# Kernel optimization log

Hardware: AMD Instinct MI355X
Metric: run time of the kernel (lower is better)

The kernel has to match this reference:

```python
import jax, jax.numpy as jnp
from jax import lax
import numpy as np

D_MODEL = 512
MODES = 16
B, S = 8, 4096
EPS = 1e-5


def setup_inputs() -> dict:
    key = jax.random.key(0)
    ks = jax.random.split(key, 7)
    x = jax.random.normal(ks[0], (B, S, D_MODEL), dtype=jnp.float32)
    gamma = jnp.ones((D_MODEL,), dtype=jnp.float32)
    beta = jnp.zeros((D_MODEL,), dtype=jnp.float32)
    # complex spectral weights stored as real/imag parts, torch init: randn(cfloat)*0.02
    wr = jax.random.normal(ks[1], (D_MODEL, MODES), dtype=jnp.float32) * 0.02
    wi = jax.random.normal(ks[2], (D_MODEL, MODES), dtype=jnp.float32) * 0.02
    # Conv1d(d_model, d_model, 3): weight (out, in, k), torch default uniform(-b, b)
    bound = 1.0 / np.sqrt(D_MODEL * 3)
    conv_w = jax.random.uniform(ks[3], (D_MODEL, D_MODEL, 3), dtype=jnp.float32, minval=-bound, maxval=bound)
    conv_b = jax.random.uniform(ks[4], (D_MODEL,), dtype=jnp.float32, minval=-bound, maxval=bound)
    return {"x": x, "gamma": gamma, "beta": beta, "wr": wr, "wi": wi,
            "conv_w": conv_w, "conv_b": conv_b}


def reference(x, gamma, beta, wr, wi, conv_w, conv_b):
    Bq, Sq, Dq = x.shape
    residual = x
    # LayerNorm over last dim (biased variance, eps=1e-5)
    mu = jnp.mean(x, axis=-1, keepdims=True)
    var = jnp.var(x, axis=-1, keepdims=True)
    xn = (x - mu) * lax.rsqrt(var + EPS) * gamma + beta
    # truncated-mode spectral conv: rfft along seq, multiply first `modes` bins, irfft
    xf = jnp.fft.rfft(xn, axis=1, norm='ortho')           # [B, S//2+1, D] complex
    m = min(wr.shape[1], xf.shape[1])
    w = (wr + 1j * wi).T[:m]                              # [m, D]
    out_ft = jnp.zeros_like(xf).at[:, :m, :].set(xf[:, :m, :] * w[None])
    xs = jnp.fft.irfft(out_ft, n=Sq, axis=1, norm='ortho')  # [B, S, D] real
    # Conv1d(k=3, pad=1) over seq dim on channel-first layout
    xc = lax.conv_general_dilated(
        xs.transpose(0, 2, 1), conv_w, window_strides=(1,), padding=[(1, 1)],
        dimension_numbers=('NCH', 'OIH', 'NCH'))
    xc = (xc + conv_b[None, :, None]).transpose(0, 2, 1)
    return residual + xs + xc
```

## Files before the change

kernel.cpp:

```cpp
#include <hip/hip_runtime.h>
#include <hip/hip_bf16.h>
#include <math.h>

#define Bn 8
#define Sn 4096
#define Dn 512
#define MODES 16
#define ANGF 0.0015339807878856412f

#define PART_OFF 0
#define Y_OFF 8388608
#define WTF_OFF 8519680
#define ZP_OFF 9306112
#define G_OFF 10878976
#define V_OFF 11010048
#define STATS_OFF 11018240

__global__ __launch_bounds__(256) void k_transpose_w(
    const float* __restrict__ cw, float* __restrict__ wTf) {
  int idx = blockIdx.x * 256 + threadIdx.x;
  int o = idx & 511;
  int d = (idx >> 9) & 511;
  int t = idx >> 18;
  wTf[idx] = cw[o * 1536 + d * 3 + t];
}

__global__ __launch_bounds__(256) void k_stats(const float* __restrict__ x,
                                               float2* __restrict__ stats) {
  int wave = threadIdx.x >> 6, lane = threadIdx.x & 63;
  int row0 = blockIdx.x * 32 + wave * 8;
  for (int j = 0; j < 8; ++j) {
    int row = row0 + j;
    const float4* px = (const float4*)(x + ((size_t)row << 9));
    float4 v0 = px[lane * 2];
    float4 v1 = px[lane * 2 + 1];
    float ps = v0.x + v0.y + v0.z + v0.w + v1.x + v1.y + v1.z + v1.w;
    float pq = v0.x * v0.x + v0.y * v0.y + v0.z * v0.z + v0.w * v0.w +
               v1.x * v1.x + v1.y * v1.y + v1.z * v1.z + v1.w * v1.w;
#pragma unroll
    for (int off = 32; off > 0; off >>= 1) {
      ps += __shfl_down(ps, off);
      pq += __shfl_down(pq, off);
    }
    if (lane == 0) {
      float mu = ps * (1.0f / Dn);
      float var = pq * (1.0f / Dn) - mu * mu;
      stats[row] = make_float2(mu, rsqrtf(var + 1e-5f));
    }
  }
}

__global__ __launch_bounds__(256) void k_project(
    const float* __restrict__ x, const float* __restrict__ gamma,
    const float* __restrict__ beta, const float2* __restrict__ stats,
    float* __restrict__ partials) {
  int blk = blockIdx.x;
  int b = blk >> 6;
  int c = blk & 63;
  int tid = threadIdx.x;
  int d0 = tid << 1;
  int s_base = c << 4;

  __shared__ __attribute__((aligned(16))) float2 s_tw[16][MODES];
  __shared__ float2 s_mv[64];
  {
    int r = tid >> 4, k = tid & 15;
    int m = ((s_base + r) * k) & (Sn - 1);
    float sn, cn;
    __sincosf((float)m * ANGF, &sn, &cn);
    s_tw[r][k] = make_float2(cn, sn);
    if (tid < 64) {
      s_mv[tid] = stats[(b << 12) + ((tid >> 4) << 10) + s_base + (tid & 15)];
    }
  }
  __syncthreads();

  float2 g = *(const float2*)(gamma + d0);
  float2 be = *(const float2*)(beta + d0);

  float2 accRe[MODES], accIm[MODES];
#pragma unroll
  for (int k = 0; k < MODES; k++) {
    accRe[k] = make_float2(0.f, 0.f);
    accIm[k] = make_float2(0.f, 0.f);
  }

  const float* xb = x + (((size_t)b << 12) << 9) + d0;
  float2 cur[4], nxt[4];
#pragma unroll
  for (int j = 0; j < 4; ++j)
    cur[j] = *(const float2*)(xb + ((size_t)((j << 10) + s_base) << 9));

#pragma unroll 2
  for (int r = 0; r < 16; ++r) {
    if (r < 15) {
#pragma unroll
      for (int j = 0; j < 4; ++j)
        nxt[j] =
            *(const float2*)(xb + ((size_t)((j << 10) + s_base + r + 1) << 9));
    }
    float2 xn[4];
#pragma unroll
    for (int j = 0; j < 4; ++j) {
      float2 mv = s_mv[(j << 4) + r];
      float ax = mv.y * g.x, ay = mv.y * g.y;
      xn[j] = make_float2((cur[j].x - mv.x) * ax + be.x,
                          (cur[j].y - mv.x) * ay + be.y);
    }
    float2 t02p = make_float2(xn[0].x + xn[2].x, xn[0].y + xn[2].y);
    float2 t02m = make_float2(xn[0].x - xn[2].x, xn[0].y - xn[2].y);
    float2 t13p = make_float2(xn[1].x + xn[3].x, xn[1].y + xn[3].y);
    float2 t13m = make_float2(xn[1].x - xn[3].x, xn[1].y - xn[3].y);
    float2 u0 = make_float2(t02p.x + t13p.x, t02p.y + t13p.y);
    float2 u1 = make_float2(t02p.x - t13p.x, t02p.y - t13p.y);

    const float4* twr = (const float4*)&s_tw[r][0];
#pragma unroll
    for (int kk = 0; kk < 8; ++kk) {
      float4 t2 = twr[kk];
      const int k0 = 2 * kk, k1 = 2 * kk + 1;
      {
        float2 u = ((k0 & 3) == 0) ? u0 : u1;
        accRe[k0].x += u.x * t2.x;
        accRe[k0].y += u.y * t2.x;
        accIm[k0].x -= u.x * t2.y;
        accIm[k0].y -= u.y * t2.y;
      }
      if ((k1 & 3) == 1) {
        accRe[k1].x += t2.z * t02m.x - t2.w * t13m.x;
        accRe[k1].y += t2.z * t02m.y - t2.w * t13m.y;
        accIm[k1].x -= t2.z * t13m.x + t2.w * t02m.x;
        accIm[k1].y -= t2.z * t13m.y + t2.w * t02m.y;
      } else {
        accRe[k1].x += t2.z * t02m.x + t2.w * t13m.x;
        accRe[k1].y += t2.z * t02m.y + t2.w * t13m.y;
        accIm[k1].x += t2.z * t13m.x - t2.w * t02m.x;
        accIm[k1].y += t2.z * t13m.y - t2.w * t02m.y;
      }
    }
#pragma unroll
    for (int j = 0; j < 4; ++j) cur[j] = nxt[j];
  }

  size_t base = ((size_t)(b * 64 + c)) * MODES;
  float4* P4 = (float4*)partials;
#pragma unroll
  for (int k = 0; k < MODES; k++)
    P4[(base + k) * 256 + tid] =
        make_float4(accRe[k].x, accIm[k].x, accRe[k].y, accIm[k].y);
}

__global__ __launch_bounds__(256) void k_reduce_modes(
    const float* __restrict__ partials, const float* __restrict__ wr,
    const float* __restrict__ wi, float* __restrict__ Y) {
  int idx = blockIdx.x * 256 + threadIdx.x;
  int d = idx & 511;
  int k = (idx >> 9) & 15;
  int b = idx >> 13;
  const float2* P = (const float2*)partials;
  float re = 0.f, im = 0.f;
#pragma unroll 8
  for (int c = 0; c < 64; c++) {
    float2 p = P[(((size_t)(b * 64 + c)) * MODES + k) * Dn + d];
    re += p.x;
    im += p.y;
  }
  float wrv = wr[d * MODES + k];
  float wiv = wi[d * MODES + k];
  float yre = re * wrv - im * wiv;
  float yim = re * wiv + im * wrv;
  float scale = (k == 0) ? (1.0f / 4096.0f) : (2.0f / 4096.0f);
  ((float2*)Y)[((size_t)b * MODES + k) * Dn + d] =
      make_float2(yre * scale, yim * scale);
}

__global__ __launch_bounds__(256) void k_build_z(
    const float* __restrict__ Y, const float* __restrict__ wTf,
    float* __restrict__ Zp) {
  int blk = blockIdx.x;
  int b = blk / 96;
  int rem = blk % 96;
  int t = rem >> 5;
  int r2 = rem & 31;
  int och = r2 >> 2;
  int dch = r2 & 3;
  int tid = threadIdx.x;
  int oi = tid & 63, kq = tid >> 6;
  int o = och * 64 + oi;
  int d0 = dch * 128;

  __shared__ float2 Ys[MODES][128];
  const float2* Y2 = (const float2*)Y;
#pragma unroll
  for (int i = 0; i < 8; i++) {
    int e = tid + i * 256;
    int k = e >> 7, dd = e & 127;
    Ys[k][dd] = Y2[(((size_t)(b * MODES + k)) << 9) + d0 + dd];
  }
  __syncthreads();

  float zc[4] = {0.f, 0.f, 0.f, 0.f}, zs[4] = {0.f, 0.f, 0.f, 0.f};
  const float* wp = wTf + (((size_t)(t * Dn + d0)) << 9) + o;
  float wv_n = wp[0];
  for (int dd = 0; dd < 128; ++dd) {
    float wv = wv_n;
    if (dd < 127) wv_n = wp[(size_t)(dd + 1) << 9];
#pragma unroll
    for (int m = 0; m < 4; m++) {
      float2 y = Ys[kq * 4 + m][dd];
      zc[m] += y.x * wv;
      zs[m] += y.y * wv;
    }
  }
  float2* Z2 = (float2*)Zp;
#pragma unroll
  for (int m = 0; m < 4; m++) {
    int k = kq * 4 + m;
    Z2[(((size_t)(dch * 24 + b * 3 + t) * MODES + k)) << 9 | o] =
        make_float2(zc[m], zs[m]);
  }
}

__global__ __launch_bounds__(256) void k_build_g(
    const float* __restrict__ Y, const float* __restrict__ Zp,
    float* __restrict__ G, float* __restrict__ V) {
  int idx = blockIdx.x * 256 + threadIdx.x;
  const float2* Y2 = (const float2*)Y;
  const float2* Z2 = (const float2*)Zp;
  if (idx < 65536) {
    int o = idx & 511;
    int k = (idx >> 9) & 15;
    int b = idx >> 13;
    float2 z0 = make_float2(0.f, 0.f), z1 = z0, z2 = z0;
#pragma unroll
    for (int dch = 0; dch < 4; dch++) {
      float2 a0 = Z2[(((size_t)(dch * 24 + b * 3 + 0) * MODES + k)) << 9 | o];
      float2 a1 = Z2[(((size_t)(dch * 24 + b * 3 + 1) * MODES + k)) << 9 | o];
      float2 a2 = Z2[(((size_t)(dch * 24 + b * 3 + 2) * MODES + k)) << 9 | o];
      z0.x += a0.x; z0.y += a0.y;
      z1.x += a1.x; z1.y += a1.y;
      z2.x += a2.x; z2.y += a2.y;
    }
    float2 y = Y2[(((size_t)(b * MODES + k)) << 9) + o];
    float sf, cf;
    __sincosf((float)k * ANGF, &sf, &cf);
    float gc = y.x + (cf * z0.x + sf * z0.y) + z1.x + (cf * z2.x - sf * z2.y);
    float gs = y.y + (cf * z0.y - sf * z0.x) + z1.y + (cf * z2.y + sf * z2.x);
    G[(((size_t)(b * MODES + k) * 2 + 0)) << 9 | o] = gc;
    G[(((size_t)(b * MODES + k) * 2 + 1)) << 9 | o] = gs;
  } else if (idx < 65536 + 8192) {
    int j = idx - 65536;
    int o = j & 511;
    int comp = (j >> 9) & 1;
    int b = j >> 10;
    float v = 0.f;
#pragma unroll
    for (int k = 0; k < MODES; k++) {
      float2 z = make_float2(0.f, 0.f);
#pragma unroll
      for (int dch = 0; dch < 4; dch++) {
        float2 a = Z2[(((size_t)(dch * 24 + b * 3 + (comp ? 2 : 0)) * MODES +
                        k)) << 9 | o];
        z.x += a.x; z.y += a.y;
      }
      if (comp == 0) {
        float sf, cf;
        __sincosf((float)k * ANGF, &sf, &cf);
        v += cf * z.x + sf * z.y;
      } else {
        v += z.x;
      }
    }
    V[((size_t)(b * 2 + comp) << 9) + o] = v;
  }
}

__global__ __launch_bounds__(256) void k_apply(
    const float* __restrict__ x, const float* __restrict__ G,
    const float* __restrict__ V, const float* __restrict__ conv_b,
    float* __restrict__ out) {
  int b = blockIdx.x >> 7;
  int rt = blockIdx.x & 127;
  int r0 = rt << 3;
  int tid = threadIdx.x;
  int o0 = tid << 1;

  __shared__ __attribute__((aligned(16))) float2 s_tw[8][MODES];
  if (tid < 128) {
    int rr = tid >> 4, k = tid & 15;
    int m = ((r0 + rr) * k) & (Sn - 1);
    float sn, cn;
    __sincosf((float)m * ANGF, &sn, &cn);
    s_tw[rr][k] = make_float2(cn, sn);
  }

  float2 Gc[MODES], Gs[MODES];
  const float2* Gp = (const float2*)(G + ((size_t)b * MODES * 2 * Dn));
#pragma unroll
  for (int k = 0; k < MODES; k++) {
    Gc[k] = Gp[(k * 2 + 0) * 256 + tid];
    Gs[k] = Gp[(k * 2 + 1) * 256 + tid];
  }
  float2 cb2 = *(const float2*)&conv_b[o0];
  __syncthreads();

  const float* xb = x + (((size_t)b << 12) << 9) + o0;
  float* ob = out + (((size_t)b << 12) << 9) + o0;

  float2 cur[4], nxt[4];
#pragma unroll
  for (int j = 0; j < 4; ++j)
    cur[j] = *(const float2*)(xb + ((size_t)((j << 10) + r0) << 9));

#pragma unroll 2
  for (int rr = 0; rr < 8; ++rr) {
    if (rr < 7) {
#pragma unroll
      for (int j = 0; j < 4; ++j)
        nxt[j] = *(const float2*)(xb + ((size_t)((j << 10) + r0 + rr + 1) << 9));
    }
    float2 a0 = make_float2(0.f, 0.f), a1 = a0, a2 = a0, a3 = a0;
    const float4* twr = (const float4*)&s_tw[rr][0];
#pragma unroll
    for (int kk = 0; kk < 8; ++kk) {
      float4 t2 = twr[kk];
#define APPLY_K(kidx, cc, ss)                                          \
  {                                                                    \
    float2 Pre = make_float2(cc * Gc[kidx].x - ss * Gs[kidx].x,        \
                             cc * Gc[kidx].y - ss * Gs[kidx].y);       \
    float2 Pim = make_float2(cc * Gs[kidx].x + ss * Gc[kidx].x,        \
                             cc * Gs[kidx].y + ss * Gc[kidx].y);       \
    a0.x += Pre.x; a0.y += Pre.y;                                      \
    if (((kidx) & 3) == 0) {                                           \
      a1.x += Pre.x; a1.y += Pre.y;                                    \
      a2.x += Pre.x; a2.y += Pre.y;                                    \
      a3.x += Pre.x; a3.y += Pre.y;                                    \
    } else if (((kidx) & 3) == 1) {                                    \
      a1.x -= Pim.x; a1.y -= Pim.y;                                    \
      a2.x -= Pre.x; a2.y -= Pre.y;                                    \
      a3.x += Pim.x; a3.y += Pim.y;                                    \
    } else if (((kidx) & 3) == 2) {                                    \
      a1.x -= Pre.x; a1.y -= Pre.y;                                    \
      a2.x += Pre.x; a2.y += Pre.y;                                    \
      a3.x -= Pre.x; a3.y -= Pre.y;                                    \
    } else {                                                           \
      a1.x += Pim.x; a1.y += Pim.y;                                    \
      a2.x -= Pre.x; a2.y -= Pre.y;                                    \
      a3.x -= Pim.x; a3.y -= Pim.y;                                    \
    }                                                                  \
  }
      APPLY_K(2 * kk, t2.x, t2.y);
      APPLY_K(2 * kk + 1, t2.z, t2.w);
#undef APPLY_K
    }
    int s_r = r0 + rr;
#pragma unroll
    for (int j = 0; j < 4; ++j) {
      float2 aj = (j == 0) ? a0 : (j == 1) ? a1 : (j == 2) ? a2 : a3;
      int s = s_r + (j << 10);
      float2 o2 = make_float2(cur[j].x + cb2.x + aj.x,
                              cur[j].y + cb2.y + aj.y);
      if (s == 0) {
        float2 v = *(const float2*)&V[((size_t)(b * 2 + 0) << 9) + o0];
        o2.x -= v.x; o2.y -= v.y;
      }
      if (s == Sn - 1) {
        float2 v = *(const float2*)&V[((size_t)(b * 2 + 1) << 9) + o0];
        o2.x -= v.x; o2.y -= v.y;
      }
      *(float2*)(ob + ((size_t)s << 9)) = o2;
    }
#pragma unroll
    for (int j = 0; j < 4; ++j) cur[j] = nxt[j];
  }
}

extern "C" void kernel_launch(void* const* d_in, const int* in_sizes, int n_in,
                              void* d_out, int out_size, void* d_ws,
                              size_t ws_size, hipStream_t stream) {
  const float* x = (const float*)d_in[0];
  const float* gamma = (const float*)d_in[1];
  const float* beta = (const float*)d_in[2];
  const float* wr = (const float*)d_in[3];
  const float* wi = (const float*)d_in[4];
  const float* conv_w = (const float*)d_in[5];
  const float* conv_b = (const float*)d_in[6];
  float* out = (float*)d_out;

  float* ws = (float*)d_ws;
  float* partials = ws + PART_OFF;
  float* Y = ws + Y_OFF;
  float* wTf = ws + WTF_OFF;
  float* Zp = ws + ZP_OFF;
  float* G = ws + G_OFF;
  float* V = ws + V_OFF;
  float2* stats = (float2*)(ws + STATS_OFF);

  hipLaunchKernelGGL(k_transpose_w, dim3(3072), dim3(256), 0, stream, conv_w,
                     wTf);
  hipLaunchKernelGGL(k_stats, dim3(1024), dim3(256), 0, stream, x, stats);
  hipLaunchKernelGGL(k_project, dim3(512), dim3(256), 0, stream, x, gamma,
                     beta, stats, partials);
  hipLaunchKernelGGL(k_reduce_modes, dim3(256), dim3(256), 0, stream, partials,
                     wr, wi, Y);
  hipLaunchKernelGGL(k_build_z, dim3(768), dim3(256), 0, stream, Y, wTf, Zp);
  hipLaunchKernelGGL(k_build_g, dim3(288), dim3(256), 0, stream, Y, Zp, G, V);
  hipLaunchKernelGGL(k_apply, dim3(1024), dim3(256), 0, stream, x, G, V,
                     conv_b, out);
}
```

Before: 190.2 us.

## Fuse LayerNorm stats into projection and merge middle stages into cooperative kernel

Computes per-row LayerNorm mean and rstd inside k_project rather than in a separate k_stats pass. The weight transpose, mode reduction, Z build and G/V build are merged into one cooperative kernel that uses grid.sync between phases. This drops four kernel launches and one extra read of x, in exchange for grid-wide barriers and a cooperative launch of 768 blocks that must all be co-resident.

```diff
diff --git a/kernel.cpp b/kernel.cpp
--- a/kernel.cpp
+++ b/kernel.cpp
@@ -1,6 +1,9 @@
 #include <hip/hip_runtime.h>
 #include <hip/hip_bf16.h>
+#include <hip/hip_cooperative_groups.h>
 #include <math.h>
+
+namespace cg = cooperative_groups;
 
 #define Bn 8
 #define Sn 4096
@@ -14,46 +17,10 @@
 #define ZP_OFF 9306112
 #define G_OFF 10878976
 #define V_OFF 11010048
-#define STATS_OFF 11018240
-
-__global__ __launch_bounds__(256) void k_transpose_w(
-    const float* __restrict__ cw, float* __restrict__ wTf) {
-  int idx = blockIdx.x * 256 + threadIdx.x;
-  int o = idx & 511;
-  int d = (idx >> 9) & 511;
-  int t = idx >> 18;
-  wTf[idx] = cw[o * 1536 + d * 3 + t];
-}
-
-__global__ __launch_bounds__(256) void k_stats(const float* __restrict__ x,
-                                               float2* __restrict__ stats) {
-  int wave = threadIdx.x >> 6, lane = threadIdx.x & 63;
-  int row0 = blockIdx.x * 32 + wave * 8;
-  for (int j = 0; j < 8; ++j) {
-    int row = row0 + j;
-    const float4* px = (const float4*)(x + ((size_t)row << 9));
-    float4 v0 = px[lane * 2];
-    float4 v1 = px[lane * 2 + 1];
-    float ps = v0.x + v0.y + v0.z + v0.w + v1.x + v1.y + v1.z + v1.w;
-    float pq = v0.x * v0.x + v0.y * v0.y + v0.z * v0.z + v0.w * v0.w +
-               v1.x * v1.x + v1.y * v1.y + v1.z * v1.z + v1.w * v1.w;
-#pragma unroll
-    for (int off = 32; off > 0; off >>= 1) {
-      ps += __shfl_down(ps, off);
-      pq += __shfl_down(pq, off);
-    }
-    if (lane == 0) {
-      float mu = ps * (1.0f / Dn);
-      float var = pq * (1.0f / Dn) - mu * mu;
-      stats[row] = make_float2(mu, rsqrtf(var + 1e-5f));
-    }
-  }
-}
 
 __global__ __launch_bounds__(256) void k_project(
     const float* __restrict__ x, const float* __restrict__ gamma,
-    const float* __restrict__ beta, const float2* __restrict__ stats,
-    float* __restrict__ partials) {
+    const float* __restrict__ beta, float* __restrict__ partials) {
   int blk = blockIdx.x;
   int b = blk >> 6;
   int c = blk & 63;
@@ -63,14 +30,44 @@
 
   __shared__ __attribute__((aligned(16))) float2 s_tw[16][MODES];
   __shared__ float2 s_mv[64];
+
   {
     int r = tid >> 4, k = tid & 15;
     int m = ((s_base + r) * k) & (Sn - 1);
     float sn, cn;
     __sincosf((float)m * ANGF, &sn, &cn);
     s_tw[r][k] = make_float2(cn, sn);
-    if (tid < 64) {
-      s_mv[tid] = stats[(b << 12) + ((tid >> 4) << 10) + s_base + (tid & 15)];
+  }
+
+  {
+    int w = tid >> 6, lane = tid & 63;
+    const float4* px = (const float4*)(
+        x + (((size_t)((b << 12) + (w << 10) + s_base)) << 9));
+#pragma unroll
+    for (int rg = 0; rg < 16; rg += 4) {
+      float4 v[8];
+#pragma unroll
+      for (int q = 0; q < 4; ++q) {
+        v[2 * q] = px[(rg + q) * 128 + lane * 2];
+        v[2 * q + 1] = px[(rg + q) * 128 + lane * 2 + 1];
+      }
+#pragma unroll
+      for (int q = 0; q < 4; ++q) {
+        float4 v0 = v[2 * q], v1 = v[2 * q + 1];
+        float ps = v0.x + v0.y + v0.z + v0.w + v1.x + v1.y + v1.z + v1.w;
+        float pq = v0.x * v0.x + v0.y * v0.y + v0.z * v0.z + v0.w * v0.w +
+                   v1.x * v1.x + v1.y * v1.y + v1.z * v1.z + v1.w * v1.w;
+#pragma unroll
+        for (int off = 32; off > 0; off >>= 1) {
+          ps += __shfl_down(ps, off);
+          pq += __shfl_down(pq, off);
+        }
+        if (lane == 0) {
+          float mu = ps * (1.0f / Dn);
+          float var = pq * (1.0f / Dn) - mu * mu;
+          s_mv[w * 16 + rg + q] = make_float2(mu, rsqrtf(var + 1e-5f));
+        }
+      }
     }
   }
   __syncthreads();
@@ -150,128 +147,146 @@
         make_float4(accRe[k].x, accIm[k].x, accRe[k].y, accIm[k].y);
 }
 
-__global__ __launch_bounds__(256) void k_reduce_modes(
+__global__ __launch_bounds__(256, 3) void k_mid(
+    const float* __restrict__ cw, float* __restrict__ wTf,
     const float* __restrict__ partials, const float* __restrict__ wr,
-    const float* __restrict__ wi, float* __restrict__ Y) {
-  int idx = blockIdx.x * 256 + threadIdx.x;
-  int d = idx & 511;
-  int k = (idx >> 9) & 15;
-  int b = idx >> 13;
-  const float2* P = (const float2*)partials;
-  float re = 0.f, im = 0.f;
-#pragma unroll 8
-  for (int c = 0; c < 64; c++) {
-    float2 p = P[(((size_t)(b * 64 + c)) * MODES + k) * Dn + d];
-    re += p.x;
-    im += p.y;
-  }
-  float wrv = wr[d * MODES + k];
-  float wiv = wi[d * MODES + k];
-  float yre = re * wrv - im * wiv;
-  float yim = re * wiv + im * wrv;
-  float scale = (k == 0) ? (1.0f / 4096.0f) : (2.0f / 4096.0f);
-  ((float2*)Y)[((size_t)b * MODES + k) * Dn + d] =
-      make_float2(yre * scale, yim * scale);
-}
-
-__global__ __launch_bounds__(256) void k_build_z(
-    const float* __restrict__ Y, const float* __restrict__ wTf,
-    float* __restrict__ Zp) {
+    const float* __restrict__ wi, float* __restrict__ Y,
+    float* __restrict__ Zp, float* __restrict__ G, float* __restrict__ V) {
+  cg::grid_group grid = cg::this_grid();
   int blk = blockIdx.x;
-  int b = blk / 96;
-  int rem = blk % 96;
-  int t = rem >> 5;
-  int r2 = rem & 31;
-  int och = r2 >> 2;
-  int dch = r2 & 3;
   int tid = threadIdx.x;
-  int oi = tid & 63, kq = tid >> 6;
-  int o = och * 64 + oi;
-  int d0 = dch * 128;
 
   __shared__ float2 Ys[MODES][128];
-  const float2* Y2 = (const float2*)Y;
-#pragma unroll
-  for (int i = 0; i < 8; i++) {
-    int e = tid + i * 256;
-    int k = e >> 7, dd = e & 127;
-    Ys[k][dd] = Y2[(((size_t)(b * MODES + k)) << 9) + d0 + dd];
-  }
-  __syncthreads();
-
-  float zc[4] = {0.f, 0.f, 0.f, 0.f}, zs[4] = {0.f, 0.f, 0.f, 0.f};
-  const float* wp = wTf + (((size_t)(t * Dn + d0)) << 9) + o;
-  float wv_n = wp[0];
-  for (int dd = 0; dd < 128; ++dd) {
-    float wv = wv_n;
-    if (dd < 127) wv_n = wp[(size_t)(dd + 1) << 9];
-#pragma unroll
-    for (int m = 0; m < 4; m++) {
-      float2 y = Ys[kq * 4 + m][dd];
-      zc[m] += y.x * wv;
-      zs[m] += y.y * wv;
-    }
-  }
-  float2* Z2 = (float2*)Zp;
-#pragma unroll
-  for (int m = 0; m < 4; m++) {
-    int k = kq * 4 + m;
-    Z2[(((size_t)(dch * 24 + b * 3 + t) * MODES + k)) << 9 | o] =
-        make_float2(zc[m], zs[m]);
-  }
-}
-
-__global__ __launch_bounds__(256) void k_build_g(
-    const float* __restrict__ Y, const float* __restrict__ Zp,
-    float* __restrict__ G, float* __restrict__ V) {
-  int idx = blockIdx.x * 256 + threadIdx.x;
-  const float2* Y2 = (const float2*)Y;
-  const float2* Z2 = (const float2*)Zp;
-  if (idx < 65536) {
-    int o = idx & 511;
+
+  {
+    int base0 = blk << 10;
+#pragma unroll
+    for (int u = 0; u < 4; ++u) {
+      int idx = base0 + (u << 8) + tid;
+      int o = idx & 511;
+      int d = (idx >> 9) & 511;
+      int t = idx >> 18;
+      wTf[idx] = cw[o * 1536 + d * 3 + t];
+    }
+  }
+  if (blk < 256) {
+    int idx = (blk << 8) + tid;
+    int d = idx & 511;
     int k = (idx >> 9) & 15;
     int b = idx >> 13;
-    float2 z0 = make_float2(0.f, 0.f), z1 = z0, z2 = z0;
-#pragma unroll
-    for (int dch = 0; dch < 4; dch++) {
-      float2 a0 = Z2[(((size_t)(dch * 24 + b * 3 + 0) * MODES + k)) << 9 | o];
-      float2 a1 = Z2[(((size_t)(dch * 24 + b * 3 + 1) * MODES + k)) << 9 | o];
-      float2 a2 = Z2[(((size_t)(dch * 24 + b * 3 + 2) * MODES + k)) << 9 | o];
-      z0.x += a0.x; z0.y += a0.y;
-      z1.x += a1.x; z1.y += a1.y;
-      z2.x += a2.x; z2.y += a2.y;
-    }
-    float2 y = Y2[(((size_t)(b * MODES + k)) << 9) + o];
-    float sf, cf;
-    __sincosf((float)k * ANGF, &sf, &cf);
-    float gc = y.x + (cf * z0.x + sf * z0.y) + z1.x + (cf * z2.x - sf * z2.y);
-    float gs = y.y + (cf * z0.y - sf * z0.x) + z1.y + (cf * z2.y + sf * z2.x);
-    G[(((size_t)(b * MODES + k) * 2 + 0)) << 9 | o] = gc;
-    G[(((size_t)(b * MODES + k) * 2 + 1)) << 9 | o] = gs;
-  } else if (idx < 65536 + 8192) {
-    int j = idx - 65536;
-    int o = j & 511;
-    int comp = (j >> 9) & 1;
-    int b = j >> 10;
-    float v = 0.f;
-#pragma unroll
-    for (int k = 0; k < MODES; k++) {
-      float2 z = make_float2(0.f, 0.f);
+    const float2* P = (const float2*)partials;
+    float re = 0.f, im = 0.f;
+#pragma unroll 8
+    for (int c = 0; c < 64; c++) {
+      float2 p = P[(((size_t)(b * 64 + c)) * MODES + k) * Dn + d];
+      re += p.x;
+      im += p.y;
+    }
+    float wrv = wr[d * MODES + k];
+    float wiv = wi[d * MODES + k];
+    float yre = re * wrv - im * wiv;
+    float yim = re * wiv + im * wrv;
+    float scale = (k == 0) ? (1.0f / 4096.0f) : (2.0f / 4096.0f);
+    ((float2*)Y)[((size_t)b * MODES + k) * Dn + d] =
+        make_float2(yre * scale, yim * scale);
+  }
+
+  grid.sync();
+
+  {
+    int b = blk / 96;
+    int rem = blk % 96;
+    int t = rem >> 5;
+    int r2 = rem & 31;
+    int och = r2 >> 2;
+    int dch = r2 & 3;
+    int oi = tid & 63, kq = tid >> 6;
+    int o = och * 64 + oi;
+    int d0 = dch * 128;
+
+    const float2* Y2 = (const float2*)Y;
+#pragma unroll
+    for (int i = 0; i < 8; i++) {
+      int e = tid + i * 256;
+      int k = e >> 7, dd = e & 127;
+      Ys[k][dd] = Y2[(((size_t)(b * MODES + k)) << 9) + d0 + dd];
+    }
+    __syncthreads();
+
+    float zc[4] = {0.f, 0.f, 0.f, 0.f}, zs[4] = {0.f, 0.f, 0.f, 0.f};
+    const float* wp = wTf + (((size_t)(t * Dn + d0)) << 9) + o;
+    float wv_n = wp[0];
+    for (int dd = 0; dd < 128; ++dd) {
+      float wv = wv_n;
+      if (dd < 127) wv_n = wp[(size_t)(dd + 1) << 9];
+#pragma unroll
+      for (int m = 0; m < 4; m++) {
+        float2 y = Ys[kq * 4 + m][dd];
+        zc[m] += y.x * wv;
+        zs[m] += y.y * wv;
+      }
+    }
+    float2* Z2 = (float2*)Zp;
+#pragma unroll
+    for (int m = 0; m < 4; m++) {
+      int k = kq * 4 + m;
+      Z2[(((size_t)(dch * 24 + b * 3 + t) * MODES + k)) << 9 | o] =
+          make_float2(zc[m], zs[m]);
+    }
+  }
+
+  grid.sync();
+
+  {
+    int idx = (blk << 8) + tid;
+    const float2* Y2 = (const float2*)Y;
+    const float2* Z2 = (const float2*)Zp;
+    if (idx < 65536) {
+      int o = idx & 511;
+      int k = (idx >> 9) & 15;
+      int b = idx >> 13;
+      float2 z0 = make_float2(0.f, 0.f), z1 = z0, z2 = z0;
 #pragma unroll
       for (int dch = 0; dch < 4; dch++) {
-        float2 a = Z2[(((size_t)(dch * 24 + b * 3 + (comp ? 2 : 0)) * MODES +
-                        k)) << 9 | o];
-        z.x += a.x; z.y += a.y;
-      }
-      if (comp == 0) {
-        float sf, cf;
-        __sincosf((float)k * ANGF, &sf, &cf);
-        v += cf * z.x + sf * z.y;
-      } else {
-        v += z.x;
-      }
-    }
-    V[((size_t)(b * 2 + comp) << 9) + o] = v;
+        float2 a0 = Z2[(((size_t)(dch * 24 + b * 3 + 0) * MODES + k)) << 9 | o];
+        float2 a1 = Z2[(((size_t)(dch * 24 + b * 3 + 1) * MODES + k)) << 9 | o];
+        float2 a2 = Z2[(((size_t)(dch * 24 + b * 3 + 2) * MODES + k)) << 9 | o];
+        z0.x += a0.x; z0.y += a0.y;
+        z1.x += a1.x; z1.y += a1.y;
+        z2.x += a2.x; z2.y += a2.y;
+      }
+      float2 y = Y2[(((size_t)(b * MODES + k)) << 9) + o];
+      float sf, cf;
+      __sincosf((float)k * ANGF, &sf, &cf);
+      float gc = y.x + (cf * z0.x + sf * z0.y) + z1.x + (cf * z2.x - sf * z2.y);
+      float gs = y.y + (cf * z0.y - sf * z0.x) + z1.y + (cf * z2.y + sf * z2.x);
+      G[(((size_t)(b * MODES + k) * 2 + 0)) << 9 | o] = gc;
+      G[(((size_t)(b * MODES + k) * 2 + 1)) << 9 | o] = gs;
+    } else if (idx < 65536 + 8192) {
+      int j = idx - 65536;
+      int o = j & 511;
+      int comp = (j >> 9) & 1;
+      int b = j >> 10;
+      float v = 0.f;
+#pragma unroll
+      for (int k = 0; k < MODES; k++) {
+        float2 z = make_float2(0.f, 0.f);
+#pragma unroll
+        for (int dch = 0; dch < 4; dch++) {
+          float2 a = Z2[(((size_t)(dch * 24 + b * 3 + (comp ? 2 : 0)) * MODES +
+                          k)) << 9 | o];
+          z.x += a.x; z.y += a.y;
+        }
+        if (comp == 0) {
+          float sf, cf;
+          __sincosf((float)k * ANGF, &sf, &cf);
+          v += cf * z.x + sf * z.y;
+        } else {
+          v += z.x;
+        }
+      }
+      V[((size_t)(b * 2 + comp) << 9) + o] = v;
+    }
   }
 }
 
@@ -394,17 +409,27 @@
   float* Zp = ws + ZP_OFF;
   float* G = ws + G_OFF;
   float* V = ws + V_OFF;
-  float2* stats = (float2*)(ws + STATS_OFF);
-
-  hipLaunchKernelGGL(k_transpose_w, dim3(3072), dim3(256), 0, stream, conv_w,
-                     wTf);
-  hipLaunchKernelGGL(k_stats, dim3(1024), dim3(256), 0, stream, x, stats);
+
   hipLaunchKernelGGL(k_project, dim3(512), dim3(256), 0, stream, x, gamma,
-                     beta, stats, partials);
-  hipLaunchKernelGGL(k_reduce_modes, dim3(256), dim3(256), 0, stream, partials,
-                     wr, wi, Y);
-  hipLaunchKernelGGL(k_build_z, dim3(768), dim3(256), 0, stream, Y, wTf, Zp);
-  hipLaunchKernelGGL(k_build_g, dim3(288), dim3(256), 0, stream, Y, Zp, G, V);
+                     beta, partials);
+
+  {
+    const float* cw_a = conv_w;
+    float* wTf_a = wTf;
+    const float* part_a = partials;
+    const float* wr_a = wr;
+    const float* wi_a = wi;
+    float* Y_a = Y;
+    float* Zp_a = Zp;
+    float* G_a = G;
+    float* V_a = V;
+    void* args[] = {(void*)&cw_a, (void*)&wTf_a, (void*)&part_a,
+                    (void*)&wr_a, (void*)&wi_a,  (void*)&Y_a,
+                    (void*)&Zp_a, (void*)&G_a,   (void*)&V_a};
+    hipLaunchCooperativeKernel((const void*)k_mid, dim3(768), dim3(256), args,
+                               0, stream);
+  }
+
   hipLaunchKernelGGL(k_apply, dim3(1024), dim3(256), 0, stream, x, G, V,
                      conv_b, out);
 }
```

After: 376.8 us. +98.1%, slower.

## Fuse stats, weight transpose and G-build into neighbouring kernels

Applied to the files above, without the earlier changes.

Folds the LayerNorm statistics into k_project, which now computes the mean and rstd of its own 64 rows from x instead of reading a separate stats buffer. Extra blocks in k_project also do the conv weight transpose. k_build_z now loops over all four d-chunks itself, so it writes a single Z with no partials. The G and V build moves into k_apply, which computes them from Y and Z in registers. Together this cuts the launch count from seven to four and drops one full read pass over x, at the cost of fewer blocks in build_z and redundant G computation in every k_apply block.

```diff
diff --git a/kernel.cpp b/kernel.cpp
--- a/kernel.cpp
+++ b/kernel.cpp
@@ -11,66 +11,73 @@
 #define PART_OFF 0
 #define Y_OFF 8388608
 #define WTF_OFF 8519680
-#define ZP_OFF 9306112
-#define G_OFF 10878976
-#define V_OFF 11010048
-#define STATS_OFF 11018240
-
-__global__ __launch_bounds__(256) void k_transpose_w(
-    const float* __restrict__ cw, float* __restrict__ wTf) {
-  int idx = blockIdx.x * 256 + threadIdx.x;
-  int o = idx & 511;
-  int d = (idx >> 9) & 511;
-  int t = idx >> 18;
-  wTf[idx] = cw[o * 1536 + d * 3 + t];
-}
-
-__global__ __launch_bounds__(256) void k_stats(const float* __restrict__ x,
-                                               float2* __restrict__ stats) {
-  int wave = threadIdx.x >> 6, lane = threadIdx.x & 63;
-  int row0 = blockIdx.x * 32 + wave * 8;
-  for (int j = 0; j < 8; ++j) {
-    int row = row0 + j;
-    const float4* px = (const float4*)(x + ((size_t)row << 9));
-    float4 v0 = px[lane * 2];
-    float4 v1 = px[lane * 2 + 1];
-    float ps = v0.x + v0.y + v0.z + v0.w + v1.x + v1.y + v1.z + v1.w;
-    float pq = v0.x * v0.x + v0.y * v0.y + v0.z * v0.z + v0.w * v0.w +
-               v1.x * v1.x + v1.y * v1.y + v1.z * v1.z + v1.w * v1.w;
-#pragma unroll
-    for (int off = 32; off > 0; off >>= 1) {
-      ps += __shfl_down(ps, off);
-      pq += __shfl_down(pq, off);
-    }
-    if (lane == 0) {
-      float mu = ps * (1.0f / Dn);
-      float var = pq * (1.0f / Dn) - mu * mu;
-      stats[row] = make_float2(mu, rsqrtf(var + 1e-5f));
-    }
-  }
-}
+#define Z_OFF 9306112
 
 __global__ __launch_bounds__(256) void k_project(
     const float* __restrict__ x, const float* __restrict__ gamma,
-    const float* __restrict__ beta, const float2* __restrict__ stats,
-    float* __restrict__ partials) {
+    const float* __restrict__ beta, const float* __restrict__ cw,
+    float* __restrict__ wTf, float* __restrict__ partials) {
   int blk = blockIdx.x;
+  int tid = threadIdx.x;
+
+  if (blk >= 512) {
+    int base0 = (blk - 512) * 3072;
+#pragma unroll
+    for (int u = 0; u < 12; ++u) {
+      int idx = base0 + (u << 8) + tid;
+      int o = idx & 511;
+      int d = (idx >> 9) & 511;
+      int t = idx >> 18;
+      wTf[idx] = cw[o * 1536 + d * 3 + t];
+    }
+    return;
+  }
+
   int b = blk >> 6;
   int c = blk & 63;
-  int tid = threadIdx.x;
   int d0 = tid << 1;
   int s_base = c << 4;
 
   __shared__ __attribute__((aligned(16))) float2 s_tw[16][MODES];
   __shared__ float2 s_mv[64];
+
   {
     int r = tid >> 4, k = tid & 15;
     int m = ((s_base + r) * k) & (Sn - 1);
     float sn, cn;
     __sincosf((float)m * ANGF, &sn, &cn);
     s_tw[r][k] = make_float2(cn, sn);
-    if (tid < 64) {
-      s_mv[tid] = stats[(b << 12) + ((tid >> 4) << 10) + s_base + (tid & 15)];
+  }
+
+  {
+    int w = tid >> 6, lane = tid & 63;
+    const float4* px = (const float4*)(
+        x + (((size_t)((b << 12) + (w << 10) + s_base)) << 9));
+#pragma unroll
+    for (int rg = 0; rg < 16; rg += 4) {
+      float4 v[8];
+#pragma unroll
+      for (int q = 0; q < 4; ++q) {
+        v[2 * q] = px[(rg + q) * 128 + lane * 2];
+        v[2 * q + 1] = px[(rg + q) * 128 + lane * 2 + 1];
+      }
+#pragma unroll
+      for (int q = 0; q < 4; ++q) {
+        float4 v0 = v[2 * q], v1 = v[2 * q + 1];
+        float ps = v0.x + v0.y + v0.z + v0.w + v1.x + v1.y + v1.z + v1.w;
+        float pq = v0.x * v0.x + v0.y * v0.y + v0.z * v0.z + v0.w * v0.w +
+                   v1.x * v1.x + v1.y * v1.y + v1.z * v1.z + v1.w * v1.w;
+#pragma unroll
+        for (int off = 32; off > 0; off >>= 1) {
+          ps += __shfl_down(ps, off);
+          pq += __shfl_down(pq, off);
+        }
+        if (lane == 0) {
+          float mu = ps * (1.0f / Dn);
+          float var = pq * (1.0f / Dn) - mu * mu;
+          s_mv[w * 16 + rg + q] = make_float2(mu, rsqrtf(var + 1e-5f));
+        }
+      }
     }
   }
   __syncthreads();
@@ -176,108 +183,57 @@
 
 __global__ __launch_bounds__(256) void k_build_z(
     const float* __restrict__ Y, const float* __restrict__ wTf,
-    float* __restrict__ Zp) {
+    float* __restrict__ Z) {
   int blk = blockIdx.x;
-  int b = blk / 96;
-  int rem = blk % 96;
-  int t = rem >> 5;
-  int r2 = rem & 31;
-  int och = r2 >> 2;
-  int dch = r2 & 3;
+  int b = blk / 24;
+  int rem = blk % 24;
+  int t = rem >> 3;
+  int och = rem & 7;
   int tid = threadIdx.x;
   int oi = tid & 63, kq = tid >> 6;
   int o = och * 64 + oi;
-  int d0 = dch * 128;
 
   __shared__ float2 Ys[MODES][128];
   const float2* Y2 = (const float2*)Y;
-#pragma unroll
-  for (int i = 0; i < 8; i++) {
-    int e = tid + i * 256;
-    int k = e >> 7, dd = e & 127;
-    Ys[k][dd] = Y2[(((size_t)(b * MODES + k)) << 9) + d0 + dd];
-  }
-  __syncthreads();
 
   float zc[4] = {0.f, 0.f, 0.f, 0.f}, zs[4] = {0.f, 0.f, 0.f, 0.f};
-  const float* wp = wTf + (((size_t)(t * Dn + d0)) << 9) + o;
-  float wv_n = wp[0];
-  for (int dd = 0; dd < 128; ++dd) {
-    float wv = wv_n;
-    if (dd < 127) wv_n = wp[(size_t)(dd + 1) << 9];
-#pragma unroll
-    for (int m = 0; m < 4; m++) {
-      float2 y = Ys[kq * 4 + m][dd];
-      zc[m] += y.x * wv;
-      zs[m] += y.y * wv;
-    }
-  }
-  float2* Z2 = (float2*)Zp;
+  for (int dch = 0; dch < 4; ++dch) {
+    int d0 = dch * 128;
+#pragma unroll
+    for (int i = 0; i < 8; i++) {
+      int e = tid + i * 256;
+      int k = e >> 7, dd = e & 127;
+      Ys[k][dd] = Y2[(((size_t)(b * MODES + k)) << 9) + d0 + dd];
+    }
+    __syncthreads();
+
+    const float* wp = wTf + (((size_t)(t * Dn + d0)) << 9) + o;
+    float wv_n = wp[0];
+    for (int dd = 0; dd < 128; ++dd) {
+      float wv = wv_n;
+      if (dd < 127) wv_n = wp[(size_t)(dd + 1) << 9];
+#pragma unroll
+      for (int m = 0; m < 4; m++) {
+        float2 y = Ys[kq * 4 + m][dd];
+        zc[m] += y.x * wv;
+        zs[m] += y.y * wv;
+      }
+    }
+    __syncthreads();
+  }
+
+  float2* Z2 = (float2*)Z;
 #pragma unroll
   for (int m = 0; m < 4; m++) {
     int k = kq * 4 + m;
-    Z2[(((size_t)(dch * 24 + b * 3 + t) * MODES + k)) << 9 | o] =
+    Z2[(((size_t)((b * 3 + t) * MODES + k)) << 9) + o] =
         make_float2(zc[m], zs[m]);
   }
 }
 
-__global__ __launch_bounds__(256) void k_build_g(
-    const float* __restrict__ Y, const float* __restrict__ Zp,
-    float* __restrict__ G, float* __restrict__ V) {
-  int idx = blockIdx.x * 256 + threadIdx.x;
-  const float2* Y2 = (const float2*)Y;
-  const float2* Z2 = (const float2*)Zp;
-  if (idx < 65536) {
-    int o = idx & 511;
-    int k = (idx >> 9) & 15;
-    int b = idx >> 13;
-    float2 z0 = make_float2(0.f, 0.f), z1 = z0, z2 = z0;
-#pragma unroll
-    for (int dch = 0; dch < 4; dch++) {
-      float2 a0 = Z2[(((size_t)(dch * 24 + b * 3 + 0) * MODES + k)) << 9 | o];
-      float2 a1 = Z2[(((size_t)(dch * 24 + b * 3 + 1) * MODES + k)) << 9 | o];
-      float2 a2 = Z2[(((size_t)(dch * 24 + b * 3 + 2) * MODES + k)) << 9 | o];
-      z0.x += a0.x; z0.y += a0.y;
-      z1.x += a1.x; z1.y += a1.y;
-      z2.x += a2.x; z2.y += a2.y;
-    }
-    float2 y = Y2[(((size_t)(b * MODES + k)) << 9) + o];
-    float sf, cf;
-    __sincosf((float)k * ANGF, &sf, &cf);
-    float gc = y.x + (cf * z0.x + sf * z0.y) + z1.x + (cf * z2.x - sf * z2.y);
-    float gs = y.y + (cf * z0.y - sf * z0.x) + z1.y + (cf * z2.y + sf * z2.x);
-    G[(((size_t)(b * MODES + k) * 2 + 0)) << 9 | o] = gc;
-    G[(((size_t)(b * MODES + k) * 2 + 1)) << 9 | o] = gs;
-  } else if (idx < 65536 + 8192) {
-    int j = idx - 65536;
-    int o = j & 511;
-    int comp = (j >> 9) & 1;
-    int b = j >> 10;
-    float v = 0.f;
-#pragma unroll
-    for (int k = 0; k < MODES; k++) {
-      float2 z = make_float2(0.f, 0.f);
-#pragma unroll
-      for (int dch = 0; dch < 4; dch++) {
-        float2 a = Z2[(((size_t)(dch * 24 + b * 3 + (comp ? 2 : 0)) * MODES +
-                        k)) << 9 | o];
-        z.x += a.x; z.y += a.y;
-      }
-      if (comp == 0) {
-        float sf, cf;
-        __sincosf((float)k * ANGF, &sf, &cf);
-        v += cf * z.x + sf * z.y;
-      } else {
-        v += z.x;
-      }
-    }
-    V[((size_t)(b * 2 + comp) << 9) + o] = v;
-  }
-}
-
 __global__ __launch_bounds__(256) void k_apply(
-    const float* __restrict__ x, const float* __restrict__ G,
-    const float* __restrict__ V, const float* __restrict__ conv_b,
+    const float* __restrict__ x, const float* __restrict__ Y,
+    const float* __restrict__ Z, const float* __restrict__ conv_b,
     float* __restrict__ out) {
   int b = blockIdx.x >> 7;
   int rt = blockIdx.x & 127;
@@ -295,11 +251,33 @@
   }
 
   float2 Gc[MODES], Gs[MODES];
-  const float2* Gp = (const float2*)(G + ((size_t)b * MODES * 2 * Dn));
-#pragma unroll
-  for (int k = 0; k < MODES; k++) {
-    Gc[k] = Gp[(k * 2 + 0) * 256 + tid];
-    Gs[k] = Gp[(k * 2 + 1) * 256 + tid];
+  float v0x = 0.f, v0y = 0.f, v1x = 0.f, v1y = 0.f;
+  {
+    const float4* Y4 = (const float4*)(Y + (((size_t)b * MODES) << 10));
+    const float4* Z4 = (const float4*)(Z + (((size_t)b * 3 * MODES) << 10));
+#pragma unroll
+    for (int k = 0; k < MODES; k++) {
+      float sf, cf;
+      __sincosf((float)k * ANGF, &sf, &cf);
+      float4 z0 = Z4[((0 * MODES + k) << 8) + tid];
+      float4 z1 = Z4[((1 * MODES + k) << 8) + tid];
+      float4 z2 = Z4[((2 * MODES + k) << 8) + tid];
+      float4 y = Y4[(k << 8) + tid];
+      float r0x = cf * z0.x + sf * z0.y;
+      float i0x = cf * z0.y - sf * z0.x;
+      float r2x = cf * z2.x - sf * z2.y;
+      float i2x = cf * z2.y + sf * z2.x;
+      Gc[k].x = y.x + r0x + z1.x + r2x;
+      Gs[k].x = y.y + i0x + z1.y + i2x;
+      float r0y = cf * z0.z + sf * z0.w;
+      float i0y = cf * z0.w - sf * z0.z;
+      float r2y = cf * z2.z - sf * z2.w;
+      float i2y = cf * z2.w + sf * z2.z;
+      Gc[k].y = y.z + r0y + z1.z + r2y;
+      Gs[k].y = y.w + i0y + z1.w + i2y;
+      v0x += r0x; v0y += r0y;
+      v1x += z2.x; v1y += z2.z;
+    }
   }
   float2 cb2 = *(const float2*)&conv_b[o0];
   __syncthreads();
@@ -360,14 +338,8 @@
       int s = s_r + (j << 10);
       float2 o2 = make_float2(cur[j].x + cb2.x + aj.x,
                               cur[j].y + cb2.y + aj.y);
-      if (s == 0) {
-        float2 v = *(const float2*)&V[((size_t)(b * 2 + 0) << 9) + o0];
-        o2.x -= v.x; o2.y -= v.y;
-      }
-      if (s == Sn - 1) {
-        float2 v = *(const float2*)&V[((size_t)(b * 2 + 1) << 9) + o0];
-        o2.x -= v.x; o2.y -= v.y;
-      }
+      if (s == 0) { o2.x -= v0x; o2.y -= v0y; }
+      if (s == Sn - 1) { o2.x -= v1x; o2.y -= v1y; }
       *(float2*)(ob + ((size_t)s << 9)) = o2;
     }
 #pragma unroll
@@ -391,20 +363,13 @@
   float* partials = ws + PART_OFF;
   float* Y = ws + Y_OFF;
   float* wTf = ws + WTF_OFF;
-  float* Zp = ws + ZP_OFF;
-  float* G = ws + G_OFF;
-  float* V = ws + V_OFF;
-  float2* stats = (float2*)(ws + STATS_OFF);
-
-  hipLaunchKernelGGL(k_transpose_w, dim3(3072), dim3(256), 0, stream, conv_w,
-                     wTf);
-  hipLaunchKernelGGL(k_stats, dim3(1024), dim3(256), 0, stream, x, stats);
-  hipLaunchKernelGGL(k_project, dim3(512), dim3(256), 0, stream, x, gamma,
-                     beta, stats, partials);
+  float* Z = ws + Z_OFF;
+
+  hipLaunchKernelGGL(k_project, dim3(768), dim3(256), 0, stream, x, gamma,
+                     beta, conv_w, wTf, partials);
   hipLaunchKernelGGL(k_reduce_modes, dim3(256), dim3(256), 0, stream, partials,
                      wr, wi, Y);
-  hipLaunchKernelGGL(k_build_z, dim3(768), dim3(256), 0, stream, Y, wTf, Zp);
-  hipLaunchKernelGGL(k_build_g, dim3(288), dim3(256), 0, stream, Y, Zp, G, V);
-  hipLaunchKernelGGL(k_apply, dim3(1024), dim3(256), 0, stream, x, G, V,
+  hipLaunchKernelGGL(k_build_z, dim3(192), dim3(256), 0, stream, Y, wTf, Z);
+  hipLaunchKernelGGL(k_apply, dim3(1024), dim3(256), 0, stream, x, Y, Z,
                      conv_b, out);
 }
```

New measurement: 206.0 us. 1.08x slower.
